# Performance work log

Hardware: AMD Instinct MI355X
Metric: run time of the kernel (lower is better)

Reference implementation:

```python
import jax, jax.numpy as jnp
import numpy as np

DIM = 768
NUM_HEADS = 12
HEAD_DIM = DIM // NUM_HEADS
EPS = 1e-5


def setup_inputs() -> dict:
    key = jax.random.key(0)
    ks = jax.random.split(key, 6)
    s = 1.0 / np.sqrt(DIM)
    return {
        "x": jax.random.normal(ks[0], (8, 1024, DIM), dtype=jnp.float32),
        "qkv_w": jax.random.uniform(ks[1], (3 * DIM, DIM), jnp.float32, -s, s),
        "qkv_b": jax.random.uniform(ks[2], (3 * DIM,), jnp.float32, -s, s),
        "proj_w": jax.random.uniform(ks[3], (DIM, DIM), jnp.float32, -s, s),
        "proj_b": jax.random.uniform(ks[4], (DIM,), jnp.float32, -s, s),
        "qn_gamma": jnp.ones((HEAD_DIM,), jnp.float32),
        "qn_beta": jnp.zeros((HEAD_DIM,), jnp.float32),
    }


def _layernorm(x, gamma, beta):
    mu = jnp.mean(x, axis=-1, keepdims=True)
    var = jnp.var(x, axis=-1, keepdims=True)
    return (x - mu) * jax.lax.rsqrt(var + EPS) * gamma + beta


def reference(x, qkv_w, qkv_b, proj_w, proj_b, qn_gamma, qn_beta):
    B, N, D = x.shape
    scale = HEAD_DIM ** -0.5
    qkv = x @ qkv_w.T + qkv_b  # [B, N, 3*D]
    qkv = qkv.reshape(B, N, 3, NUM_HEADS, HEAD_DIM).transpose(2, 0, 3, 1, 4)
    q, k, v = qkv[0], qkv[1], qkv[2]  # each [B, H, N, hd]
    # Original code applies q_norm to BOTH q and k (faithful to source).
    q = _layernorm(q, qn_gamma, qn_beta)
    k = _layernorm(k, qn_gamma, qn_beta)
    scores = jnp.einsum("bhqd,bhkd->bhqk", q, k) * scale  # [B, H, N, N]
    attn = jax.nn.softmax(scores, axis=-1)
    out = jnp.einsum("bhqk,bhkd->bhqd", attn, v)  # [B, H, N, hd]
    out = out.transpose(0, 2, 1, 3).reshape(B, N, D)
    return out @ proj_w.T + proj_b
```

## Files before the change

### kernel.cpp

```cpp
#include <hip/hip_runtime.h>
#include <stdint.h>

#define DIM   768
#define NHEAD 12
#define HD    64
#define BATCH 8
#define SEQ   1024
#define MROWS (BATCH * SEQ)
#define EPSLN 1e-5f
#define QK_SCALE (0.125f * 1.44269504f)

typedef __attribute__((ext_vector_type(8))) short s8v;
typedef __attribute__((ext_vector_type(4))) short s4v;
typedef __attribute__((ext_vector_type(4))) float f32x4;

__device__ inline short f2bf(float f) {
    union { float f; unsigned u; } v; v.f = f;
    unsigned r = v.u + 0x7FFFu + ((v.u >> 16) & 1u);
    return (short)(r >> 16);
}
__device__ inline unsigned pk2bf(float lo, float hi) {
    union { float f; unsigned u; } a, b; a.f = lo; b.f = hi;
    return __builtin_amdgcn_perm(b.u + 0x8000u, a.u + 0x8000u, 0x07060302u);
}
__device__ inline void gload16(const void* g, void* l) {
    __builtin_amdgcn_global_load_lds(
        (const __attribute__((address_space(1))) void*)g,
        (__attribute__((address_space(3))) void*)l, 16, 0, 0);
}

#define N4_X (MROWS * DIM / 4)
#define N4_W1 (3 * DIM * DIM / 4)
#define N4_W2 (DIM * DIM / 4)
__global__ __launch_bounds__(256) void cvt_all(
    const float* __restrict__ x, const float* __restrict__ w1,
    const float* __restrict__ w2, short* __restrict__ dx,
    short* __restrict__ dw1, short* __restrict__ dw2)
{
    size_t i = (size_t)blockIdx.x * 256 + threadIdx.x;
    const float* s; short* d;
    if (i < N4_X)                { s = x  + i * 4;               d = dx  + i * 4; }
    else if (i < N4_X + N4_W1)   { size_t j = i - N4_X;          s = w1 + j * 4; d = dw1 + j * 4; }
    else                         { size_t j = i - N4_X - N4_W1;  s = w2 + j * 4; d = dw2 + j * 4; }
    float4 v = *(const float4*)s;
    uint2 o; o.x = pk2bf(v.x, v.y); o.y = pk2bf(v.z, v.w);
    *(uint2*)d = o;
}

template<int BM>
__global__ __launch_bounds__(256) void gemm_mfma(
    const short* __restrict__ A, const short* __restrict__ W,
    const float* __restrict__ bias,
    short* __restrict__ oq, short* __restrict__ ok, short* __restrict__ ov,
    float* __restrict__ oplain, int Ncols, int qkv_mode,
    const float* __restrict__ gamma, const float* __restrict__ beta)
{
    constexpr int MT = BM / 32;
    __shared__ __align__(16) short As[2][BM * 64];
    __shared__ __align__(16) short Bs[2][128 * 64];

    const int tid  = threadIdx.x;
    const int gx    = gridDim.x;
    const int id    = blockIdx.y * gx + blockIdx.x;
    const int chunk = (gx * gridDim.y) >> 3;
    const int vid   = (id & 7) * chunk + (id >> 3);
    const int m0   = (vid / gx) * BM;
    const int n0   = (vid % gx) * 128;
    const int w    = tid >> 6, lane = tid & 63;
    const int quad = lane >> 4, l16 = lane & 15;
    const int wm   = (w & 1) * (BM / 2), wn = (w >> 1) * 64;
    const int rsw  = l16 & 7;

    f32x4 acc[MT][4];
#pragma unroll
    for (int i = 0; i < MT; ++i)
#pragma unroll
        for (int j = 0; j < 4; ++j) acc[i][j] = (f32x4){0.f, 0.f, 0.f, 0.f};

    auto stage = [&](int buf, int k0) {
#pragma unroll
        for (int i = 0; i < BM / 32; ++i) {
            int f   = i * 256 + tid;
            int row = f >> 3;
            int c   = (f & 7) ^ (row & 7);
            gload16(&A[(size_t)(m0 + row) * DIM + k0 + c * 8], &As[buf][f * 8]);
        }
#pragma unroll
        for (int i = 0; i < 4; ++i) {
            int f   = i * 256 + tid;
            int row = f >> 3;
            int c   = (f & 7) ^ (row & 7);
            gload16(&W[(size_t)(n0 + row) * DIM + k0 + c * 8], &Bs[buf][f * 8]);
        }
    };

    constexpr int NK = DIM / 64;
    stage(0, 0);
    __syncthreads();

    for (int t = 0; t < NK; ++t) {
        const int cur = t & 1;
        if (t + 1 < NK) stage(cur ^ 1, (t + 1) * 64);
#pragma unroll
        for (int ks = 0; ks < 2; ++ks) {
            const int ch = ((ks * 4 + quad) ^ rsw) * 8;
            s8v af[MT], bw[4];
#pragma unroll
            for (int t2 = 0; t2 < MT; ++t2)
                af[t2] = *(const s8v*)&As[cur][(wm + t2 * 16 + l16) * 64 + ch];
#pragma unroll
            for (int t2 = 0; t2 < 4; ++t2)
                bw[t2] = *(const s8v*)&Bs[cur][(wn + t2 * 16 + l16) * 64 + ch];
#pragma unroll
            for (int mt = 0; mt < MT; ++mt)
#pragma unroll
                for (int nt = 0; nt < 4; ++nt)
                    acc[mt][nt] = __builtin_amdgcn_mfma_f32_16x16x32_bf16(
                        af[mt], bw[nt], acc[mt][nt], 0, 0, 0);
        }
        __syncthreads();
    }

    if (qkv_mode) {
        const int which = n0 / DIM;
        if (which == 2) {
#pragma unroll
            for (int mt = 0; mt < MT; ++mt)
#pragma unroll
                for (int nt = 0; nt < 4; ++nt)
#pragma unroll
                    for (int i = 0; i < 4; ++i) {
                        int m  = m0 + wm + mt * 16 + quad * 4 + i;
                        int n  = n0 + wn + nt * 16 + l16;
                        float cv = acc[mt][nt][i] + bias[n];
                        int bb = m >> 10, nn = m & 1023;
                        int d  = n - 2 * DIM;
                        int hh = d >> 6, e = d & 63;
                        ov[(((size_t)(bb * NHEAD + hh)) * HD + e) * SEQ + nn] = f2bf(cv);
                    }
        } else {
            const float qs = (which == 0) ? QK_SCALE : 1.0f;
            short* dst = which ? ok : oq;
            const int hh = (n0 + wn - which * DIM) >> 6;
            float ge[4], be[4];
#pragma unroll
            for (int nt = 0; nt < 4; ++nt) {
                ge[nt] = gamma[nt * 16 + l16];
                be[nt] = beta [nt * 16 + l16] * qs;
            }
#pragma unroll
            for (int mt = 0; mt < MT; ++mt)
#pragma unroll
                for (int i = 0; i < 4; ++i) {
                    float cv[4], s = 0.f, s2 = 0.f;
#pragma unroll
                    for (int nt = 0; nt < 4; ++nt) {
                        int n = n0 + wn + nt * 16 + l16;
                        cv[nt] = acc[mt][nt][i] + bias[n];
                        s  += cv[nt];
                        s2 += cv[nt] * cv[nt];
                    }
                    s  += __shfl_xor(s, 1);  s  += __shfl_xor(s, 2);
                    s  += __shfl_xor(s, 4);  s  += __shfl_xor(s, 8);
                    s2 += __shfl_xor(s2, 1); s2 += __shfl_xor(s2, 2);
                    s2 += __shfl_xor(s2, 4); s2 += __shfl_xor(s2, 8);
                    float mu  = s * (1.f / 64.f);
                    float var = s2 * (1.f / 64.f) - mu * mu;
                    float rs  = rsqrtf(var + EPSLN) * qs;
                    int m  = m0 + wm + mt * 16 + quad * 4 + i;
                    int bb = m >> 10, nn = m & 1023;
                    short* rp = &dst[(((size_t)(bb * NHEAD + hh)) * SEQ + nn) * HD];
#pragma unroll
                    for (int nt = 0; nt < 4; ++nt) {
                        float val = (cv[nt] - mu) * rs * ge[nt] + be[nt];
                        rp[nt * 16 + l16] = f2bf(val);
                    }
                }
        }
    } else {
#pragma unroll
        for (int mt = 0; mt < MT; ++mt)
#pragma unroll
            for (int nt = 0; nt < 4; ++nt)
#pragma unroll
                for (int i = 0; i < 4; ++i) {
                    int m = m0 + wm + mt * 16 + quad * 4 + i;
                    int n = n0 + wn + nt * 16 + l16;
                    oplain[(size_t)m * Ncols + n] = acc[mt][nt][i] + bias[n];
                }
    }
}

__global__ __launch_bounds__(256) void attn_mfma(
    const short* __restrict__ q, const short* __restrict__ k,
    const short* __restrict__ vt, short* __restrict__ O)
{
    const int id   = blockIdx.y * gridDim.x + blockIdx.x;
    const int vid  = (id & 7) * 192 + (id >> 3);
    const int bh   = vid >> 4;
    const int q0   = (vid & 15) * 64;
    const int b    = bh / NHEAD;
    const int h    = bh % NHEAD;
    const int tid  = threadIdx.x;
    const int w    = tid >> 6;
    const int lane = tid & 63;
    const int quad = lane >> 4;
    const int l16  = lane & 15;

    __shared__ __align__(16) char smem[22528];
    __shared__ float denom[4][64];

    short (*Pw)[44]   = (short(*)[44])(smem + (size_t)w * (64 * 44 * 2));
    float (*Obuf)[68] = (float(*)[68])smem;

    const size_t base   = (size_t)bh * SEQ * HD;
    const size_t vtbase = (size_t)bh * HD * SEQ;

    s8v qB[4][2];
#pragma unroll
    for (int qt = 0; qt < 4; ++qt)
#pragma unroll
        for (int hf = 0; hf < 2; ++hf)
            qB[qt][hf] = *(const s8v*)&q[base + (size_t)(q0 + qt * 16 + l16) * HD
                                         + hf * 32 + quad * 8];

    f32x4 oacc[4][4];
    float lacc[4] = {0.f, 0.f, 0.f, 0.f};
#pragma unroll
    for (int a = 0; a < 4; ++a)
#pragma unroll
        for (int c = 0; c < 4; ++c) oacc[a][c] = (f32x4){0.f, 0.f, 0.f, 0.f};

    auto loadK = [&](s8v (&kd)[2][2], int kb2) {
#pragma unroll
        for (int kt = 0; kt < 2; ++kt)
#pragma unroll
            for (int hf = 0; hf < 2; ++hf)
                kd[kt][hf] = *(const s8v*)&k[base + (size_t)(kb2 + kt * 16 + l16) * HD
                                             + hf * 32 + quad * 8];
    };

    auto body = [&](int jb, s8v (&kc)[2][2], s8v (&kn)[2][2], bool pre) {
        const int kb = jb * 128 + w * 32;

        s8v va[4];
#pragma unroll
        for (int et = 0; et < 4; ++et)
            va[et] = *(const s8v*)&vt[vtbase + (size_t)(et * 16 + l16) * SEQ
                                      + kb + quad * 8];
        if (pre) loadK(kn, kb + 128);

#pragma unroll
        for (int qt = 0; qt < 4; ++qt)
#pragma unroll
            for (int kt = 0; kt < 2; ++kt) {
                f32x4 c = (f32x4){0.f, 0.f, 0.f, 0.f};
                c = __builtin_amdgcn_mfma_f32_16x16x32_bf16(kc[kt][0], qB[qt][0], c, 0, 0, 0);
                c = __builtin_amdgcn_mfma_f32_16x16x32_bf16(kc[kt][1], qB[qt][1], c, 0, 0, 0);
                float p0 = exp2f(c[0]), p1 = exp2f(c[1]);
                float p2 = exp2f(c[2]), p3 = exp2f(c[3]);
                lacc[qt] += (p0 + p1) + (p2 + p3);
                uint2 pk; pk.x = pk2bf(p0, p1); pk.y = pk2bf(p2, p3);
                *(uint2*)&Pw[qt * 16 + l16][kt * 16 + quad * 4] = pk;
            }

        s8v pb[4];
#pragma unroll
        for (int qt = 0; qt < 4; ++qt)
            pb[qt] = *(const s8v*)&Pw[qt * 16 + l16][quad * 8];

        __builtin_amdgcn_s_setprio(1);
#pragma unroll
        for (int et = 0; et < 4; ++et)
#pragma unroll
            for (int qt = 0; qt < 4; ++qt)
                oacc[et][qt] = __builtin_amdgcn_mfma_f32_16x16x32_bf16(
                    va[et], pb[qt], oacc[et][qt], 0, 0, 0);
        __builtin_amdgcn_s_setprio(0);
    };

    s8v kA0[2][2], kA1[2][2];
    loadK(kA0, w * 32);
    for (int jp = 0; jp < 4; ++jp) {
        body(jp * 2,     kA0, kA1, true);
        body(jp * 2 + 1, kA1, kA0, jp < 3);
    }

#pragma unroll
    for (int qt = 0; qt < 4; ++qt) {
        float s = lacc[qt];
        s += __shfl_xor(s, 16);
        s += __shfl_xor(s, 32);
        denom[w][qt * 16 + l16] = s;
    }
    __syncthreads();

    for (int r = 0; r < 4; ++r) {
        if (w == r) {
#pragma unroll
            for (int et = 0; et < 4; ++et)
#pragma unroll
                for (int qt = 0; qt < 4; ++qt) {
                    float* dst = &Obuf[qt * 16 + l16][et * 16 + quad * 4];
                    float4 ov;
                    if (r == 0) ov = make_float4(0.f, 0.f, 0.f, 0.f);
                    else        ov = *(float4*)dst;
                    ov.x += oacc[et][qt][0]; ov.y += oacc[et][qt][1];
                    ov.z += oacc[et][qt][2]; ov.w += oacc[et][qt][3];
                    *(float4*)dst = ov;
                }
        }
        __syncthreads();
    }

    const int qq = tid >> 2;
    const int e0 = (tid & 3) * 16;
    float linv = 1.0f / (denom[0][qq] + denom[1][qq] + denom[2][qq] + denom[3][qq]);
    float4 f0 = *(float4*)&Obuf[qq][e0];
    float4 f1 = *(float4*)&Obuf[qq][e0 + 4];
    float4 f2 = *(float4*)&Obuf[qq][e0 + 8];
    float4 f3 = *(float4*)&Obuf[qq][e0 + 12];
    short* op = &O[((size_t)b * SEQ + q0 + qq) * DIM + h * HD + e0];
    uint4 o1, o2;
    o1.x = pk2bf(f0.x * linv, f0.y * linv);
    o1.y = pk2bf(f0.z * linv, f0.w * linv);
    o1.z = pk2bf(f1.x * linv, f1.y * linv);
    o1.w = pk2bf(f1.z * linv, f1.w * linv);
    o2.x = pk2bf(f2.x * linv, f2.y * linv);
    o2.y = pk2bf(f2.z * linv, f2.w * linv);
    o2.z = pk2bf(f3.x * linv, f3.y * linv);
    o2.w = pk2bf(f3.z * linv, f3.w * linv);
    *(uint4*)&op[0] = o1;
    *(uint4*)&op[8] = o2;
}

extern "C" void kernel_launch(void* const* d_in, const int* in_sizes, int n_in,
                              void* d_out, int out_size, void* d_ws, size_t ws_size,
                              hipStream_t stream)
{
    const float* x      = (const float*)d_in[0];
    const float* qkv_w  = (const float*)d_in[1];
    const float* qkv_b  = (const float*)d_in[2];
    const float* proj_w = (const float*)d_in[3];
    const float* proj_b = (const float*)d_in[4];
    const float* gamma  = (const float*)d_in[5];
    const float* beta   = (const float*)d_in[6];
    float* out = (float*)d_out;

    const size_t PER = (size_t)BATCH * NHEAD * SEQ * HD;
    short* qb  = (short*)d_ws;
    short* kb  = qb + PER;
    short* vtb = kb + PER;
    short* ob  = vtb + PER;
    short* xb  = ob + PER;
    short* wqb = xb + (size_t)MROWS * DIM;
    short* wpb = wqb + (size_t)3 * DIM * DIM;

    cvt_all<<<dim3((N4_X + N4_W1 + N4_W2) / 256), 256, 0, stream>>>(
        x, qkv_w, proj_w, xb, wqb, wpb);

    gemm_mfma<128><<<dim3(2304 / 128, MROWS / 128), 256, 0, stream>>>(
        xb, wqb, qkv_b, qb, kb, vtb, nullptr, 2304, 1, gamma, beta);

    attn_mfma<<<dim3(SEQ / 64, BATCH * NHEAD), 256, 0, stream>>>(
        qb, kb, vtb, ob);

    gemm_mfma<64><<<dim3(DIM / 128, MROWS / 64), 256, 0, stream>>>(
        ob, wpb, proj_b, nullptr, nullptr, nullptr, out, DIM, 0, nullptr, nullptr);
}
```

Measured before the change: 214.3 us.

## Software-pipeline attention: overlap PV MFMAs with next block's QK and exp

Restructures the attention inner loop so the PV matrix multiply for the previous key block is interleaved with the QK^T MFMAs and exp2 work for the current block. V and the P fragments are carried over in registers, with a final epilogue doing the last PV. The goal is to hide exp and transcendental latency behind matrix-core work. The GEMM also drops its grouped block-index swizzle in favour of direct blockIdx mapping, which may change L2 reuse. Carrying extra fragments raises register pressure, and reusing the shared P buffer relies on each wave reading P before overwriting it.

```diff
diff --git a/kernel.cpp b/kernel.cpp
--- a/kernel.cpp
+++ b/kernel.cpp
@@ -60,12 +60,8 @@
     __shared__ __align__(16) short Bs[2][128 * 64];
 
     const int tid  = threadIdx.x;
-    const int gx    = gridDim.x;
-    const int id    = blockIdx.y * gx + blockIdx.x;
-    const int chunk = (gx * gridDim.y) >> 3;
-    const int vid   = (id & 7) * chunk + (id >> 3);
-    const int m0   = (vid / gx) * BM;
-    const int n0   = (vid % gx) * 128;
+    const int m0   = blockIdx.y * BM;
+    const int n0   = blockIdx.x * 128;
     const int w    = tid >> 6, lane = tid & 63;
     const int quad = lane >> 4, l16 = lane & 15;
     const int wm   = (w & 1) * (BM / 2), wn = (w >> 1) * 64;
@@ -239,52 +235,68 @@
                 kd[kt][hf] = *(const s8v*)&k[base + (size_t)(kb2 + kt * 16 + l16) * HD
                                              + hf * 32 + quad * 8];
     };
-
-    auto body = [&](int jb, s8v (&kc)[2][2], s8v (&kn)[2][2], bool pre) {
-        const int kb = jb * 128 + w * 32;
-
-        s8v va[4];
+    auto loadV = [&](s8v (&vd)[4], int kb2) {
 #pragma unroll
         for (int et = 0; et < 4; ++et)
-            va[et] = *(const s8v*)&vt[vtbase + (size_t)(et * 16 + l16) * SEQ
-                                      + kb + quad * 8];
-        if (pre) loadK(kn, kb + 128);
-
-#pragma unroll
-        for (int qt = 0; qt < 4; ++qt)
-#pragma unroll
-            for (int kt = 0; kt < 2; ++kt) {
-                f32x4 c = (f32x4){0.f, 0.f, 0.f, 0.f};
-                c = __builtin_amdgcn_mfma_f32_16x16x32_bf16(kc[kt][0], qB[qt][0], c, 0, 0, 0);
-                c = __builtin_amdgcn_mfma_f32_16x16x32_bf16(kc[kt][1], qB[qt][1], c, 0, 0, 0);
-                float p0 = exp2f(c[0]), p1 = exp2f(c[1]);
-                float p2 = exp2f(c[2]), p3 = exp2f(c[3]);
-                lacc[qt] += (p0 + p1) + (p2 + p3);
-                uint2 pk; pk.x = pk2bf(p0, p1); pk.y = pk2bf(p2, p3);
-                *(uint2*)&Pw[qt * 16 + l16][kt * 16 + quad * 4] = pk;
-            }
-
-        s8v pb[4];
+            vd[et] = *(const s8v*)&vt[vtbase + (size_t)(et * 16 + l16) * SEQ
+                                      + kb2 + quad * 8];
+    };
+    auto readPB = [&](s8v (&pb)[4]) {
 #pragma unroll
         for (int qt = 0; qt < 4; ++qt)
             pb[qt] = *(const s8v*)&Pw[qt * 16 + l16][quad * 8];
-
+    };
+
+    s8v kA[2][2], kB[2][2];
+    s8v vP[4], pbP[4];
+
+    auto mix = [&](int jb, s8v (&kc)[2][2], s8v (&kn)[2][2], bool dopv, bool prek) {
+        const int kb = jb * 128 + w * 32;
+        if (prek) loadK(kn, kb + 128);
         __builtin_amdgcn_s_setprio(1);
 #pragma unroll
-        for (int et = 0; et < 4; ++et)
-#pragma unroll
-            for (int qt = 0; qt < 4; ++qt)
-                oacc[et][qt] = __builtin_amdgcn_mfma_f32_16x16x32_bf16(
-                    va[et], pb[qt], oacc[et][qt], 0, 0, 0);
+        for (int i8 = 0; i8 < 8; ++i8) {
+            const int qt = i8 >> 1, kt = i8 & 1;
+            f32x4 c = (f32x4){0.f, 0.f, 0.f, 0.f};
+            c = __builtin_amdgcn_mfma_f32_16x16x32_bf16(kc[kt][0], qB[qt][0], c, 0, 0, 0);
+            c = __builtin_amdgcn_mfma_f32_16x16x32_bf16(kc[kt][1], qB[qt][1], c, 0, 0, 0);
+            if (dopv) {
+                const int et = i8 >> 1;
+                const int q2 = (i8 & 1) * 2;
+                oacc[et][q2]     = __builtin_amdgcn_mfma_f32_16x16x32_bf16(
+                    vP[et], pbP[q2],     oacc[et][q2],     0, 0, 0);
+                oacc[et][q2 + 1] = __builtin_amdgcn_mfma_f32_16x16x32_bf16(
+                    vP[et], pbP[q2 + 1], oacc[et][q2 + 1], 0, 0, 0);
+            }
+            float p0 = exp2f(c[0]), p1 = exp2f(c[1]);
+            float p2 = exp2f(c[2]), p3 = exp2f(c[3]);
+            lacc[qt] += (p0 + p1) + (p2 + p3);
+            uint2 pk; pk.x = pk2bf(p0, p1); pk.y = pk2bf(p2, p3);
+            *(uint2*)&Pw[qt * 16 + l16][kt * 16 + quad * 4] = pk;
+        }
         __builtin_amdgcn_s_setprio(0);
-    };
-
-    s8v kA0[2][2], kA1[2][2];
-    loadK(kA0, w * 32);
-    for (int jp = 0; jp < 4; ++jp) {
-        body(jp * 2,     kA0, kA1, true);
-        body(jp * 2 + 1, kA1, kA0, jp < 3);
-    }
+        loadV(vP, kb);
+        readPB(pbP);
+    };
+
+    loadK(kA, w * 32);
+    mix(0, kA, kB, false, true);
+    mix(1, kB, kA, true,  true);
+    mix(2, kA, kB, true,  true);
+    mix(3, kB, kA, true,  true);
+    mix(4, kA, kB, true,  true);
+    mix(5, kB, kA, true,  true);
+    mix(6, kA, kB, true,  true);
+    mix(7, kB, kA, true,  false);
+
+    __builtin_amdgcn_s_setprio(1);
+#pragma unroll
+    for (int et = 0; et < 4; ++et)
+#pragma unroll
+        for (int qt = 0; qt < 4; ++qt)
+            oacc[et][qt] = __builtin_amdgcn_mfma_f32_16x16x32_bf16(
+                vP[et], pbP[qt], oacc[et][qt], 0, 0, 0);
+    __builtin_amdgcn_s_setprio(0);
 
 #pragma unroll
     for (int qt = 0; qt < 4; ++qt) {
```

Result: slower. 219.4 us (+2.4%).
